# Kernel optimization log

Hardware: AMD Instinct MI355X
Metric: run time of the kernel (lower is better)

## Reference

```python
import jax, jax.numpy as jnp
import numpy as np

H = 2048          # hidden_size
I = 768           # moe_intermediate_size
E = 64            # num_experts
TOP_K = 8         # num_experts_per_tok (norm_topk_prob=True)
B, S = 1, 1024


def setup_inputs() -> dict:
    key = jax.random.key(0)
    ks = jax.random.split(key, 5)
    scale = 0.02
    return {
        "hidden_states": jax.random.normal(ks[0], (B, S, H), dtype=jnp.float32),
        "W_router": jax.random.normal(ks[1], (H, E), dtype=jnp.float32) * scale,
        "W_gate": jax.random.normal(ks[2], (E, H, I), dtype=jnp.float32) * scale,
        "W_up": jax.random.normal(ks[3], (E, H, I), dtype=jnp.float32) * scale,
        "W_down": jax.random.normal(ks[4], (E, I, H), dtype=jnp.float32) * scale,
    }


def reference(hidden_states, W_router, W_gate, W_up, W_down):
    b, s, h = hidden_states.shape
    x = hidden_states.reshape(-1, h)                      # [T, H]

    # --- Qwen3MoeTopKRouter: linear gate -> fp32 softmax -> top-k -> renorm ---
    logits = x @ W_router                                 # [T, E]
    probs = jax.nn.softmax(logits.astype(jnp.float32), axis=-1)
    top_w, top_idx = jax.lax.top_k(probs, TOP_K)          # [T, K]
    top_w = top_w / jnp.sum(top_w, axis=-1, keepdims=True)  # norm_topk_prob
    top_w = top_w.astype(x.dtype)

    # combine weights per (token, expert): zero if expert not selected
    comb = jnp.sum(jax.nn.one_hot(top_idx, E, dtype=x.dtype) * top_w[..., None], axis=1)  # [T, E]

    # --- per-expert SwiGLU MLP: down(silu(gate(x)) * up(x)), dense-masked ---
    g = jnp.einsum('th,ehi->eti', x, W_gate)              # [E, T, I]
    u = jnp.einsum('th,ehi->eti', x, W_up)                # [E, T, I]
    hmid = jax.nn.silu(g) * u                             # [E, T, I]
    # fold combine weight into the intermediate to avoid an [E, T, H] buffer
    hmid = hmid * comb.T[:, :, None]                      # [E, T, I]
    out = jnp.einsum('eti,eih->th', hmid, W_down)         # [T, H]

    return out.reshape(b, s, h)
```

## Files before the change

kernel.cpp:

```cpp
#include <hip/hip_runtime.h>
#include <hip/hip_bf16.h>

#define H_DIM 2048
#define I_DIM 768
#define NEXP 64
#define TOPK 8
#define NTOK 1024
#define BM 256
#define BKS 32

typedef float f32x4 __attribute__((ext_vector_type(4)));
typedef float f32x2 __attribute__((ext_vector_type(2)));
typedef unsigned int u32x4 __attribute__((ext_vector_type(4)));
typedef short bf16v8 __attribute__((ext_vector_type(8)));
typedef unsigned int u32;


__device__ inline unsigned short f2bf(float f) {
    union { float f; u32 u; } v; v.f = f;
    u32 r = (v.u + 0x7FFFu + ((v.u >> 16) & 1u)) >> 16;
    return (unsigned short)r;
}
__device__ inline u32 pack2(float a, float b) {
    return (u32)f2bf(a) | ((u32)f2bf(b) << 16);
}

__global__ void zero_kernel(float4* p, int n4) {
    int i = blockIdx.x * blockDim.x + threadIdx.x;
    if (i < n4) p[i] = (float4){0.f, 0.f, 0.f, 0.f};
}

__global__ void xconv_kernel(const float4* __restrict__ x, ushort4* __restrict__ xbf, int n4) {
    int i = blockIdx.x * blockDim.x + threadIdx.x;
    if (i < n4) {
        float4 v = x[i];
        ushort4 o;
        o.x = f2bf(v.x); o.y = f2bf(v.y); o.z = f2bf(v.z); o.w = f2bf(v.w);
        xbf[i] = o;
    }
}

__global__ __launch_bounds__(64) void router_kernel(
    const float* __restrict__ x, const float* __restrict__ Wr,
    int* __restrict__ topk_idx, float* __restrict__ topk_w)
{
    const int t = blockIdx.x;
    const int e = threadIdx.x;
    __shared__ float xs[H_DIM];

    const float* xrow = x + (size_t)t * H_DIM;
    #pragma unroll
    for (int m = 0; m < H_DIM / 64; ++m) xs[m * 64 + e] = xrow[m * 64 + e];
    __syncthreads();

    float acc = 0.f;
    #pragma unroll 8
    for (int h = 0; h < H_DIM; ++h) acc += xs[h] * Wr[(size_t)h * NEXP + e];

    float m = acc;
    #pragma unroll
    for (int o = 32; o > 0; o >>= 1) m = fmaxf(m, __shfl_xor(m, o));
    float p = __expf(acc - m);
    float s = p;
    #pragma unroll
    for (int o = 32; o > 0; o >>= 1) s += __shfl_xor(s, o);
    float prob = p / s;

    float myp = prob;
    float kw[TOPK]; int kid[TOPK]; float wsum = 0.f;
    #pragma unroll
    for (int k = 0; k < TOPK; ++k) {
        float v = myp; int bi = e;
        #pragma unroll
        for (int o = 32; o > 0; o >>= 1) {
            float ov = __shfl_xor(v, o);
            int   oi = __shfl_xor(bi, o);
            if (ov > v || (ov == v && oi < bi)) { v = ov; bi = oi; }
        }
        kw[k] = v; kid[k] = bi; wsum += v;
        if (e == bi) myp = -1.f;
    }
    if (e == 0) {
        float inv = 1.f / wsum;
        #pragma unroll
        for (int k = 0; k < TOPK; ++k) {
            topk_idx[t * TOPK + k] = kid[k];
            topk_w[t * TOPK + k]   = kw[k] * inv;
        }
    }
}

__global__ __launch_bounds__(64) void listbuild_kernel(
    const int* __restrict__ topk_idx, const float* __restrict__ topk_w,
    int* __restrict__ counts, int* __restrict__ lists, float* __restrict__ wlist)
{
    const int e = blockIdx.x;
    const int lane = threadIdx.x;
    int n = 0;
    for (int base = 0; base < NTOK * TOPK; base += 64) {
        int s = base + lane;
        int idx = topk_idx[s];
        bool match = (idx == e);
        unsigned long long mask = __ballot(match);
        int pre = __popcll(mask & ((1ull << lane) - 1ull));
        if (match) {
            lists[e * NTOK + n + pre] = s >> 3;
            wlist[e * NTOK + n + pre] = topk_w[s];
        }
        n += __popcll(mask);
    }
    if (lane == 0) counts[e] = n;
}

__global__ __launch_bounds__(64) void scan_kernel(
    const int* __restrict__ counts, int* __restrict__ offsets)
{
    int e = threadIdx.x;
    int v = counts[e];
    int xacc = v;
    #pragma unroll
    for (int o = 1; o < 64; o <<= 1) {
        int y = __shfl_up(xacc, o);
        if (e >= o) xacc += y;
    }
    offsets[e] = xacc - v;
}

__global__ __launch_bounds__(512) void gateup_kernel(
    const unsigned short* __restrict__ xbf,
    const float* __restrict__ Wg, const float* __restrict__ Wu,
    const int* __restrict__ counts, const int* __restrict__ offsets,
    const int* __restrict__ lists, const float* __restrict__ wlist,
    unsigned short* __restrict__ hmid)
{
    const int b  = blockIdx.x;
    const int wg = (b & 7) * 96 + (b >> 3);
    const int itile = wg % 12;
    const int e     = wg / 12;

    const int count = counts[e];
    if (count == 0) return;
    const int off = offsets[e];
    const int i0 = itile * 64;

    __shared__ unsigned short Alds[BM][40];
    __shared__ u32 Bgl[64 * 20];
    __shared__ u32 Bul[64 * 20];

    const int tid  = threadIdx.x;
    const int lane = tid & 63;
    const int wid  = tid >> 6;
    const int wm   = wid >> 1, wn = wid & 1;
    const int kb   = lane >> 4;
    const int l15  = lane & 15;

    const float* WgE = Wg + (size_t)e * H_DIM * I_DIM + i0;
    const float* WuE = Wu + (size_t)e * H_DIM * I_DIM + i0;

    const int bn  = (tid & 31) * 2;
    const int bkp = tid >> 5;
    const int ar  = tid >> 1;
    const int ah  = (tid & 1) * 16;

    for (int mstart = 0; mstart < count; mstart += BM) {
        const int pr = mstart + ar;
        const bool aact = pr < count;
        const unsigned short* xrow = xbf + (size_t)(aact ? lists[e * NTOK + pr] : 0) * H_DIM + ah;
        const bool mact = (mstart + wm * 64) < count;

        f32x4 accg[4][2], accu[4][2];
        #pragma unroll
        for (int i = 0; i < 4; ++i)
            #pragma unroll
            for (int j = 0; j < 2; ++j) {
                accg[i][j] = (f32x4){0.f, 0.f, 0.f, 0.f};
                accu[i][j] = (f32x4){0.f, 0.f, 0.f, 0.f};
            }

        u32x4 pA0, pA1;
        f32x2 g0a, g1a, u0a, u1a;
        f32x2 g0b, g1b, u0b, u1b;

#define LOADA(h)                                                                \
        if (aact) {                                                             \
            const u32x4* pa_ = (const u32x4*)(xrow + (h));                      \
            pA0 = pa_[0]; pA1 = pa_[1];                                         \
        }
#define LOADB(G0,G1,U0,U1,h)                                                    \
        {                                                                       \
            G0 = __builtin_nontemporal_load((const f32x2*)(WgE + (size_t)((h) + 2 * bkp)     * I_DIM + bn)); \
            G1 = __builtin_nontemporal_load((const f32x2*)(WgE + (size_t)((h) + 2 * bkp + 1) * I_DIM + bn)); \
            U0 = __builtin_nontemporal_load((const f32x2*)(WuE + (size_t)((h) + 2 * bkp)     * I_DIM + bn)); \
            U1 = __builtin_nontemporal_load((const f32x2*)(WuE + (size_t)((h) + 2 * bkp + 1) * I_DIM + bn)); \
        }
#define STOREA()                                                                \
        if (aact) {                                                             \
            *(u32x4*)&Alds[ar][ah]     = pA0;                                   \
            *(u32x4*)&Alds[ar][ah + 8] = pA1;                                   \
        }
#define STOREB(G0,G1,U0,U1)                                                     \
        {                                                                       \
            Bgl[(bn)     * 20 + bkp] = pack2(G0.x, G1.x);                       \
            Bgl[(bn + 1) * 20 + bkp] = pack2(G0.y, G1.y);                       \
            Bul[(bn)     * 20 + bkp] = pack2(U0.x, U1.x);                       \
            Bul[(bn + 1) * 20 + bkp] = pack2(U0.y, U1.y);                       \
        }
#define MFMA_PHASE()                                                            \
        if (mact) {                                                             \
            bf16v8 af[4], bg[2], bu[2];                                         \
            _Pragma("unroll")                                                   \
            for (int mf = 0; mf < 4; ++mf)                                      \
                af[mf] = *(const bf16v8*)&Alds[wm * 64 + mf * 16 + l15][kb * 8];\
            _Pragma("unroll")                                                   \
            for (int nf = 0; nf < 2; ++nf) {                                    \
                int n = wn * 32 + nf * 16 + l15;                                \
                bg[nf] = *(const bf16v8*)&Bgl[n * 20 + kb * 4];                 \
                bu[nf] = *(const bf16v8*)&Bul[n * 20 + kb * 4];                 \
            }                                                                   \
            _Pragma("unroll")                                                   \
            for (int mf = 0; mf < 4; ++mf)                                      \
                _Pragma("unroll")                                               \
                for (int nf = 0; nf < 2; ++nf) {                                \
                    accg[mf][nf] = __builtin_amdgcn_mfma_f32_16x16x32_bf16(af[mf], bg[nf], accg[mf][nf], 0, 0, 0); \
                    accu[mf][nf] = __builtin_amdgcn_mfma_f32_16x16x32_bf16(af[mf], bu[nf], accu[mf][nf], 0, 0, 0); \
                }                                                               \
        }

        LOADB(g0a, g1a, u0a, u1a, 0);
        LOADB(g0b, g1b, u0b, u1b, BKS);
        LOADA(0);

        for (int hh = 0; hh < H_DIM; hh += 2 * BKS) {
            STOREA(); STOREB(g0a, g1a, u0a, u1a);
            __syncthreads();
            if (hh + 2 * BKS < H_DIM) LOADB(g0a, g1a, u0a, u1a, hh + 2 * BKS);
            LOADA(hh + BKS);
            MFMA_PHASE();
            __syncthreads();
            STOREA(); STOREB(g0b, g1b, u0b, u1b);
            __syncthreads();
            if (hh + 3 * BKS < H_DIM) LOADB(g0b, g1b, u0b, u1b, hh + 3 * BKS);
            if (hh + 2 * BKS < H_DIM) LOADA(hh + 2 * BKS);
            MFMA_PHASE();
            __syncthreads();
        }
#undef LOADA
#undef LOADB
#undef STOREA
#undef STOREB
#undef MFMA_PHASE

        if (mact) {
            #pragma unroll
            for (int mf = 0; mf < 4; ++mf)
                #pragma unroll
                for (int nf = 0; nf < 2; ++nf)
                    #pragma unroll
                    for (int r = 0; r < 4; ++r) {
                        int ml  = wm * 64 + mf * 16 + (lane >> 4) * 4 + r;
                        int pos = mstart + ml;
                        if (pos < count) {
                            float wgt = wlist[e * NTOK + pos];
                            float g = accg[mf][nf][r], u = accu[mf][nf][r];
                            float s = 1.f / (1.f + __expf(-g));
                            float h = g * s * u * wgt;
                            hmid[(size_t)(off + pos) * I_DIM + i0 + wn * 32 + nf * 16 + l15] = f2bf(h);
                        }
                    }
        }
    }
}

__global__ __launch_bounds__(512) void down_kernel(
    const unsigned short* __restrict__ hmid, const float* __restrict__ Wd,
    const int* __restrict__ counts, const int* __restrict__ offsets,
    const int* __restrict__ lists, float* __restrict__ out)
{
    const int b  = blockIdx.x;
    const int wg = (b & 7) * 256 + (b >> 3);
    const int htile = wg % 32;
    const int e     = wg / 32;

    const int count = counts[e];
    if (count == 0) return;
    const int off = offsets[e];
    const int h0 = htile * 64;

    __shared__ unsigned short Alds[BM][40];
    __shared__ u32 Bdl[64 * 20];

    const int tid  = threadIdx.x;
    const int lane = tid & 63;
    const int wid  = tid >> 6;
    const int wm   = wid >> 1, wn = wid & 1;
    const int kb   = lane >> 4;
    const int l15  = lane & 15;

    const float* WdE = Wd + (size_t)e * I_DIM * H_DIM + h0;

    const int bn  = (tid & 31) * 2;
    const int bkp = tid >> 5;
    const int ar  = tid >> 1;
    const int ah  = (tid & 1) * 16;

    for (int mstart = 0; mstart < count; mstart += BM) {
        const int pr = mstart + ar;
        const bool aact = pr < count;
        const unsigned short* hrow = hmid + (size_t)(off + (aact ? pr : 0)) * I_DIM + ah;
        const bool mact = (mstart + wm * 64) < count;

        f32x4 acc[4][2];
        #pragma unroll
        for (int i = 0; i < 4; ++i)
            #pragma unroll
            for (int j = 0; j < 2; ++j) acc[i][j] = (f32x4){0.f, 0.f, 0.f, 0.f};

        u32x4 pH0, pH1;
        f32x2 d0a, d1a, d0b, d1b;

#define LOADA(k)                                                                \
        if (aact) {                                                             \
            const u32x4* p_ = (const u32x4*)(hrow + (k));                       \
            pH0 = p_[0]; pH1 = p_[1];                                           \
        }
#define LOADB(D0,D1,k)                                                          \
        {                                                                       \
            D0 = __builtin_nontemporal_load((const f32x2*)(WdE + (size_t)((k) + 2 * bkp)     * H_DIM + bn)); \
            D1 = __builtin_nontemporal_load((const f32x2*)(WdE + (size_t)((k) + 2 * bkp + 1) * H_DIM + bn)); \
        }
#define STOREA()                                                                \
        if (aact) {                                                             \
            *(u32x4*)&Alds[ar][ah]     = pH0;                                   \
            *(u32x4*)&Alds[ar][ah + 8] = pH1;                                   \
        }
#define STOREB(D0,D1)                                                           \
        {                                                                       \
            Bdl[(bn)     * 20 + bkp] = pack2(D0.x, D1.x);                       \
            Bdl[(bn + 1) * 20 + bkp] = pack2(D0.y, D1.y);                       \
        }
#define MFMA_PHASE()                                                            \
        if (mact) {                                                             \
            bf16v8 af[4], bd[2];                                                \
            _Pragma("unroll")                                                   \
            for (int mf = 0; mf < 4; ++mf)                                      \
                af[mf] = *(const bf16v8*)&Alds[wm * 64 + mf * 16 + l15][kb * 8];\
            _Pragma("unroll")                                                   \
            for (int nf = 0; nf < 2; ++nf) {                                    \
                int n = wn * 32 + nf * 16 + l15;                                \
                bd[nf] = *(const bf16v8*)&Bdl[n * 20 + kb * 4];                 \
            }                                                                   \
            _Pragma("unroll")                                                   \
            for (int mf = 0; mf < 4; ++mf)                                      \
                _Pragma("unroll")                                               \
                for (int nf = 0; nf < 2; ++nf)                                  \
                    acc[mf][nf] = __builtin_amdgcn_mfma_f32_16x16x32_bf16(af[mf], bd[nf], acc[mf][nf], 0, 0, 0); \
        }

        LOADB(d0a, d1a, 0);
        LOADB(d0b, d1b, BKS);
        LOADA(0);

        for (int ii = 0; ii < I_DIM; ii += 2 * BKS) {
            STOREA(); STOREB(d0a, d1a);
            __syncthreads();
            if (ii + 2 * BKS < I_DIM) LOADB(d0a, d1a, ii + 2 * BKS);
            LOADA(ii + BKS);
            MFMA_PHASE();
            __syncthreads();

            STOREA(); STOREB(d0b, d1b);
            __syncthreads();
            if (ii + 3 * BKS < I_DIM) LOADB(d0b, d1b, ii + 3 * BKS);
            if (ii + 2 * BKS < I_DIM) LOADA(ii + 2 * BKS);
            MFMA_PHASE();
            __syncthreads();
        }
#undef LOADA
#undef LOADB
#undef STOREA
#undef STOREB
#undef MFMA_PHASE

        if (mact) {
            #pragma unroll
            for (int mf = 0; mf < 4; ++mf)
                #pragma unroll
                for (int nf = 0; nf < 2; ++nf)
                    #pragma unroll
                    for (int r = 0; r < 4; ++r) {
                        int ml  = wm * 64 + mf * 16 + (lane >> 4) * 4 + r;
                        int pos = mstart + ml;
                        if (pos < count) {
                            int tok = lists[e * NTOK + pos];
                            atomicAdd(&out[(size_t)tok * H_DIM + h0 + wn * 32 + nf * 16 + l15],
                                      acc[mf][nf][r]);
                        }
                    }
        }
    }
}

extern "C" void kernel_launch(void* const* d_in, const int* in_sizes, int n_in,
                              void* d_out, int out_size, void* d_ws, size_t ws_size,
                              hipStream_t stream) {
    const float* x  = (const float*)d_in[0];
    const float* Wr = (const float*)d_in[1];
    const float* Wg = (const float*)d_in[2];
    const float* Wu = (const float*)d_in[3];
    const float* Wd = (const float*)d_in[4];
    float* out = (float*)d_out;

    char* ws = (char*)d_ws;
    int*   topk_idx = (int*)  (ws + 0);
    float* topk_w   = (float*)(ws + 32768);
    int*   counts   = (int*)  (ws + 65536);
    int*   offsets  = (int*)  (ws + 65792);
    int*   lists    = (int*)  (ws + 66048);
    float* wlist    = (float*)(ws + 328192);
    unsigned short* hmid = (unsigned short*)(ws + 590336);
    unsigned short* xbf  = (unsigned short*)(ws + 13173248);

    const int nout4 = NTOK * H_DIM / 4;
    hipLaunchKernelGGL(zero_kernel, dim3((nout4 + 255) / 256), dim3(256), 0, stream,
                       (float4*)out, nout4);
    hipLaunchKernelGGL(xconv_kernel, dim3((NTOK * H_DIM / 4 + 255) / 256), dim3(256), 0, stream,
                       (const float4*)x, (ushort4*)xbf, NTOK * H_DIM / 4);
    hipLaunchKernelGGL(router_kernel, dim3(NTOK), dim3(64), 0, stream,
                       x, Wr, topk_idx, topk_w);
    hipLaunchKernelGGL(listbuild_kernel, dim3(NEXP), dim3(64), 0, stream,
                       topk_idx, topk_w, counts, lists, wlist);
    hipLaunchKernelGGL(scan_kernel, dim3(1), dim3(64), 0, stream,
                       counts, offsets);
    hipLaunchKernelGGL(gateup_kernel, dim3(12 * NEXP), dim3(512), 0, stream,
                       xbf, Wg, Wu, counts, offsets, lists, wlist, hmid);
    hipLaunchKernelGGL(down_kernel, dim3(32 * NEXP), dim3(512), 0, stream,
                       hmid, Wd, counts, offsets, lists, out);
}
```

Measured before the change: 561.4 us.

## Halve N-tile width in MoE GEMMs and swizzle B LDS layout

```diff
diff --git a/kernel.cpp b/kernel.cpp
--- a/kernel.cpp
+++ b/kernel.cpp
@@ -12,6 +12,7 @@
 typedef float f32x4 __attribute__((ext_vector_type(4)));
 typedef float f32x2 __attribute__((ext_vector_type(2)));
 typedef unsigned int u32x4 __attribute__((ext_vector_type(4)));
+typedef unsigned int u32x2 __attribute__((ext_vector_type(2)));
 typedef short bf16v8 __attribute__((ext_vector_type(8)));
 typedef unsigned int u32;
 
@@ -134,18 +135,18 @@
     unsigned short* __restrict__ hmid)
 {
     const int b  = blockIdx.x;
-    const int wg = (b & 7) * 96 + (b >> 3);
-    const int itile = wg % 12;
-    const int e     = wg / 12;
+    const int wg = (b & 7) * 192 + (b >> 3);
+    const int itile = wg % 24;
+    const int e     = wg / 24;
 
     const int count = counts[e];
     if (count == 0) return;
     const int off = offsets[e];
-    const int i0 = itile * 64;
+    const int i0 = itile * 32;
 
     __shared__ unsigned short Alds[BM][40];
-    __shared__ u32 Bgl[64 * 20];
-    __shared__ u32 Bul[64 * 20];
+    __shared__ u32 Bgl[32 * 20];
+    __shared__ u32 Bul[32 * 20];
 
     const int tid  = threadIdx.x;
     const int lane = tid & 63;
@@ -157,10 +158,16 @@
     const float* WgE = Wg + (size_t)e * H_DIM * I_DIM + i0;
     const float* WuE = Wu + (size_t)e * H_DIM * I_DIM + i0;
 
-    const int bn  = (tid & 31) * 2;
-    const int bkp = tid >> 5;
-    const int ar  = tid >> 1;
-    const int ah  = (tid & 1) * 16;
+    const int ar = tid >> 1;
+    const int ah = (tid & 1) * 16;
+    const int bnn  = tid & 31;
+    const int bkq  = (tid >> 5) & 7;
+    const int bmat = tid >> 8;
+    const float* WB = bmat ? WuE : WgE;
+    const int key4w = 4 * ((bnn >> 3) & 3);
+    u32* bdst = (bmat ? Bul : Bgl) + bnn * 20 + ((2 * bkq) ^ key4w);
+    const int brn   = wn * 16 + l15;
+    const int key4r = 4 * ((brn >> 3) & 3);
 
     for (int mstart = 0; mstart < count; mstart += BM) {
         const int pr = mstart + ar;
@@ -168,78 +175,69 @@
         const unsigned short* xrow = xbf + (size_t)(aact ? lists[e * NTOK + pr] : 0) * H_DIM + ah;
         const bool mact = (mstart + wm * 64) < count;
 
-        f32x4 accg[4][2], accu[4][2];
+        f32x4 accg[4], accu[4];
         #pragma unroll
-        for (int i = 0; i < 4; ++i)
-            #pragma unroll
-            for (int j = 0; j < 2; ++j) {
-                accg[i][j] = (f32x4){0.f, 0.f, 0.f, 0.f};
-                accu[i][j] = (f32x4){0.f, 0.f, 0.f, 0.f};
-            }
+        for (int i = 0; i < 4; ++i) {
+            accg[i] = (f32x4){0.f, 0.f, 0.f, 0.f};
+            accu[i] = (f32x4){0.f, 0.f, 0.f, 0.f};
+        }
 
         u32x4 pA0, pA1;
-        f32x2 g0a, g1a, u0a, u1a;
-        f32x2 g0b, g1b, u0b, u1b;
+        float b0a, b1a, b2a, b3a;
+        float b0b, b1b, b2b, b3b;
 
 #define LOADA(h)                                                                \
         if (aact) {                                                             \
             const u32x4* pa_ = (const u32x4*)(xrow + (h));                      \
             pA0 = pa_[0]; pA1 = pa_[1];                                         \
         }
-#define LOADB(G0,G1,U0,U1,h)                                                    \
+#define LOADB(R0,R1,R2,R3,h)                                                    \
         {                                                                       \
-            G0 = __builtin_nontemporal_load((const f32x2*)(WgE + (size_t)((h) + 2 * bkp)     * I_DIM + bn)); \
-            G1 = __builtin_nontemporal_load((const f32x2*)(WgE + (size_t)((h) + 2 * bkp + 1) * I_DIM + bn)); \
-            U0 = __builtin_nontemporal_load((const f32x2*)(WuE + (size_t)((h) + 2 * bkp)     * I_DIM + bn)); \
-            U1 = __builtin_nontemporal_load((const f32x2*)(WuE + (size_t)((h) + 2 * bkp + 1) * I_DIM + bn)); \
+            R0 = __builtin_nontemporal_load(WB + (size_t)((h) + 4 * bkq)     * I_DIM + bnn); \
+            R1 = __builtin_nontemporal_load(WB + (size_t)((h) + 4 * bkq + 1) * I_DIM + bnn); \
+            R2 = __builtin_nontemporal_load(WB + (size_t)((h) + 4 * bkq + 2) * I_DIM + bnn); \
+            R3 = __builtin_nontemporal_load(WB + (size_t)((h) + 4 * bkq + 3) * I_DIM + bnn); \
         }
 #define STOREA()                                                                \
         if (aact) {                                                             \
             *(u32x4*)&Alds[ar][ah]     = pA0;                                   \
             *(u32x4*)&Alds[ar][ah + 8] = pA1;                                   \
         }
-#define STOREB(G0,G1,U0,U1)                                                     \
+#define STOREB(R0,R1,R2,R3)                                                     \
         {                                                                       \
-            Bgl[(bn)     * 20 + bkp] = pack2(G0.x, G1.x);                       \
-            Bgl[(bn + 1) * 20 + bkp] = pack2(G0.y, G1.y);                       \
-            Bul[(bn)     * 20 + bkp] = pack2(U0.x, U1.x);                       \
-            Bul[(bn + 1) * 20 + bkp] = pack2(U0.y, U1.y);                       \
+            u32x2 w_; w_.x = pack2(R0, R1); w_.y = pack2(R2, R3);               \
+            *(u32x2*)bdst = w_;                                                 \
         }
 #define MFMA_PHASE()                                                            \
         if (mact) {                                                             \
-            bf16v8 af[4], bg[2], bu[2];                                         \
+            bf16v8 af[4], bg, bu;                                               \
             _Pragma("unroll")                                                   \
             for (int mf = 0; mf < 4; ++mf)                                      \
                 af[mf] = *(const bf16v8*)&Alds[wm * 64 + mf * 16 + l15][kb * 8];\
+            bg = *(const bf16v8*)&Bgl[brn * 20 + ((4 * kb) ^ key4r)];           \
+            bu = *(const bf16v8*)&Bul[brn * 20 + ((4 * kb) ^ key4r)];           \
             _Pragma("unroll")                                                   \
-            for (int nf = 0; nf < 2; ++nf) {                                    \
-                int n = wn * 32 + nf * 16 + l15;                                \
-                bg[nf] = *(const bf16v8*)&Bgl[n * 20 + kb * 4];                 \
-                bu[nf] = *(const bf16v8*)&Bul[n * 20 + kb * 4];                 \
+            for (int mf = 0; mf < 4; ++mf) {                                    \
+                accg[mf] = __builtin_amdgcn_mfma_f32_16x16x32_bf16(af[mf], bg, accg[mf], 0, 0, 0); \
+                accu[mf] = __builtin_amdgcn_mfma_f32_16x16x32_bf16(af[mf], bu, accu[mf], 0, 0, 0); \
             }                                                                   \
-            _Pragma("unroll")                                                   \
-            for (int mf = 0; mf < 4; ++mf)                                      \
-                _Pragma("unroll")                                               \
-                for (int nf = 0; nf < 2; ++nf) {                                \
-                    accg[mf][nf] = __builtin_amdgcn_mfma_f32_16x16x32_bf16(af[mf], bg[nf], accg[mf][nf], 0, 0, 0); \
-                    accu[mf][nf] = __builtin_amdgcn_mfma_f32_16x16x32_bf16(af[mf], bu[nf], accu[mf][nf], 0, 0, 0); \
-                }                                                               \
-        }
-
-        LOADB(g0a, g1a, u0a, u1a, 0);
-        LOADB(g0b, g1b, u0b, u1b, BKS);
+        }
+
+        LOADB(b0a, b1a, b2a, b3a, 0);
+        LOADB(b0b, b1b, b2b, b3b, BKS);
         LOADA(0);
 
         for (int hh = 0; hh < H_DIM; hh += 2 * BKS) {
-            STOREA(); STOREB(g0a, g1a, u0a, u1a);
-            __syncthreads();
-            if (hh + 2 * BKS < H_DIM) LOADB(g0a, g1a, u0a, u1a, hh + 2 * BKS);
+            STOREA(); STOREB(b0a, b1a, b2a, b3a);
+            __syncthreads();
+            if (hh + 2 * BKS < H_DIM) LOADB(b0a, b1a, b2a, b3a, hh + 2 * BKS);
             LOADA(hh + BKS);
             MFMA_PHASE();
             __syncthreads();
-            STOREA(); STOREB(g0b, g1b, u0b, u1b);
-            __syncthreads();
-            if (hh + 3 * BKS < H_DIM) LOADB(g0b, g1b, u0b, u1b, hh + 3 * BKS);
+
+            STOREA(); STOREB(b0b, b1b, b2b, b3b);
+            __syncthreads();
+            if (hh + 3 * BKS < H_DIM) LOADB(b0b, b1b, b2b, b3b, hh + 3 * BKS);
             if (hh + 2 * BKS < H_DIM) LOADA(hh + 2 * BKS);
             MFMA_PHASE();
             __syncthreads();
@@ -254,19 +252,16 @@
             #pragma unroll
             for (int mf = 0; mf < 4; ++mf)
                 #pragma unroll
-                for (int nf = 0; nf < 2; ++nf)
-                    #pragma unroll
-                    for (int r = 0; r < 4; ++r) {
-                        int ml  = wm * 64 + mf * 16 + (lane >> 4) * 4 + r;
-                        int pos = mstart + ml;
-                        if (pos < count) {
-                            float wgt = wlist[e * NTOK + pos];
-                            float g = accg[mf][nf][r], u = accu[mf][nf][r];
-                            float s = 1.f / (1.f + __expf(-g));
-                            float h = g * s * u * wgt;
-                            hmid[(size_t)(off + pos) * I_DIM + i0 + wn * 32 + nf * 16 + l15] = f2bf(h);
-                        }
+                for (int r = 0; r < 4; ++r) {
+                    int pos = mstart + wm * 64 + mf * 16 + kb * 4 + r;
+                    if (pos < count) {
+                        float wgt = wlist[e * NTOK + pos];
+                        float g = accg[mf][r], u = accu[mf][r];
+                        float s = 1.f / (1.f + __expf(-g));
+                        float h = g * s * u * wgt;
+                        hmid[(size_t)(off + pos) * I_DIM + i0 + wn * 16 + l15] = f2bf(h);
                     }
+                }
         }
     }
 }
@@ -277,17 +272,17 @@
     const int* __restrict__ lists, float* __restrict__ out)
 {
     const int b  = blockIdx.x;
-    const int wg = (b & 7) * 256 + (b >> 3);
-    const int htile = wg % 32;
-    const int e     = wg / 32;
+    const int wg = (b & 7) * 512 + (b >> 3);
+    const int htile = wg % 64;
+    const int e     = wg / 64;
 
     const int count = counts[e];
     if (count == 0) return;
     const int off = offsets[e];
-    const int h0 = htile * 64;
+    const int h0 = htile * 32;
 
     __shared__ unsigned short Alds[BM][40];
-    __shared__ u32 Bdl[64 * 20];
+    __shared__ u32 Bdl[32 * 20];
 
     const int tid  = threadIdx.x;
     const int lane = tid & 63;
@@ -298,10 +293,15 @@
 
     const float* WdE = Wd + (size_t)e * I_DIM * H_DIM + h0;
 
-    const int bn  = (tid & 31) * 2;
-    const int bkp = tid >> 5;
-    const int ar  = tid >> 1;
-    const int ah  = (tid & 1) * 16;
+    const int ar = tid >> 1;
+    const int ah = (tid & 1) * 16;
+    const int bnn  = tid & 31;
+    const int bkq  = (tid >> 5) & 7;
+    const bool bact = tid < 256;
+    const int key4w = 4 * ((bnn >> 3) & 3);
+    u32* bdst = Bdl + bnn * 20 + ((2 * bkq) ^ key4w);
+    const int brn   = wn * 16 + l15;
+    const int key4r = 4 * ((brn >> 3) & 3);
 
     for (int mstart = 0; mstart < count; mstart += BM) {
         const int pr = mstart + ar;
@@ -309,68 +309,63 @@
         const unsigned short* hrow = hmid + (size_t)(off + (aact ? pr : 0)) * I_DIM + ah;
         const bool mact = (mstart + wm * 64) < count;
 
-        f32x4 acc[4][2];
+        f32x4 acc[4];
         #pragma unroll
-        for (int i = 0; i < 4; ++i)
-            #pragma unroll
-            for (int j = 0; j < 2; ++j) acc[i][j] = (f32x4){0.f, 0.f, 0.f, 0.f};
+        for (int i = 0; i < 4; ++i) acc[i] = (f32x4){0.f, 0.f, 0.f, 0.f};
 
         u32x4 pH0, pH1;
-        f32x2 d0a, d1a, d0b, d1b;
+        float d0a, d1a, d2a, d3a;
+        float d0b, d1b, d2b, d3b;
 
 #define LOADA(k)                                                                \
         if (aact) {                                                             \
             const u32x4* p_ = (const u32x4*)(hrow + (k));                       \
             pH0 = p_[0]; pH1 = p_[1];                                           \
         }
-#define LOADB(D0,D1,k)                                                          \
-        {                                                                       \
-            D0 = __builtin_nontemporal_load((const f32x2*)(WdE + (size_t)((k) + 2 * bkp)     * H_DIM + bn)); \
-            D1 = __builtin_nontemporal_load((const f32x2*)(WdE + (size_t)((k) + 2 * bkp + 1) * H_DIM + bn)); \
+#define LOADB(R0,R1,R2,R3,k)                                                    \
+        if (bact) {                                                             \
+            R0 = __builtin_nontemporal_load(WdE + (size_t)((k) + 4 * bkq)     * H_DIM + bnn); \
+            R1 = __builtin_nontemporal_load(WdE + (size_t)((k) + 4 * bkq + 1) * H_DIM + bnn); \
+            R2 = __builtin_nontemporal_load(WdE + (size_t)((k) + 4 * bkq + 2) * H_DIM + bnn); \
+            R3 = __builtin_nontemporal_load(WdE + (size_t)((k) + 4 * bkq + 3) * H_DIM + bnn); \
         }
 #define STOREA()                                                                \
         if (aact) {                                                             \
             *(u32x4*)&Alds[ar][ah]     = pH0;                                   \
             *(u32x4*)&Alds[ar][ah + 8] = pH1;                                   \
         }
-#define STOREB(D0,D1)                                                           \
-        {                                                                       \
-            Bdl[(bn)     * 20 + bkp] = pack2(D0.x, D1.x);                       \
-            Bdl[(bn + 1) * 20 + bkp] = pack2(D0.y, D1.y);                       \
+#define STOREB(R0,R1,R2,R3)                                                     \
+        if (bact) {                                                             \
+            u32x2 w_; w_.x = pack2(R0, R1); w_.y = pack2(R2, R3);               \
+            *(u32x2*)bdst = w_;                                                 \
         }
 #define MFMA_PHASE()                                                            \
         if (mact) {                                                             \
-            bf16v8 af[4], bd[2];                                                \
+            bf16v8 af[4], bd;                                                   \
             _Pragma("unroll")                                                   \
             for (int mf = 0; mf < 4; ++mf)                                      \
                 af[mf] = *(const bf16v8*)&Alds[wm * 64 + mf * 16 + l15][kb * 8];\
-            _Pragma("unroll")                                                   \
-            for (int nf = 0; nf < 2; ++nf) {                                    \
-                int n = wn * 32 + nf * 16 + l15;                                \
-                bd[nf] = *(const bf16v8*)&Bdl[n * 20 + kb * 4];                 \
-            }                                                                   \
+            bd = *(const bf16v8*)&Bdl[brn * 20 + ((4 * kb) ^ key4r)];           \
             _Pragma("unroll")                                                   \
             for (int mf = 0; mf < 4; ++mf)                                      \
-                _Pragma("unroll")                                               \
-                for (int nf = 0; nf < 2; ++nf)                                  \
-                    acc[mf][nf] = __builtin_amdgcn_mfma_f32_16x16x32_bf16(af[mf], bd[nf], acc[mf][nf], 0, 0, 0); \
-        }
-
-        LOADB(d0a, d1a, 0);
-        LOADB(d0b, d1b, BKS);
+                acc[mf] = __builtin_amdgcn_mfma_f32_16x16x32_bf16(af[mf], bd, acc[mf], 0, 0, 0); \
+        }
+
+        LOADB(d0a, d1a, d2a, d3a, 0);
+        LOADB(d0b, d1b, d2b, d3b, BKS);
         LOADA(0);
 
         for (int ii = 0; ii < I_DIM; ii += 2 * BKS) {
-            STOREA(); STOREB(d0a, d1a);
-            __syncthreads();
-            if (ii + 2 * BKS < I_DIM) LOADB(d0a, d1a, ii + 2 * BKS);
+            STOREA(); STOREB(d0a, d1a, d2a, d3a);
+            __syncthreads();
+            if (ii + 2 * BKS < I_DIM) LOADB(d0a, d1a, d2a, d3a, ii + 2 * BKS);
             LOADA(ii + BKS);
             MFMA_PHASE();
             __syncthreads();
 
-            STOREA(); STOREB(d0b, d1b);
-            __syncthreads();
-            if (ii + 3 * BKS < I_DIM) LOADB(d0b, d1b, ii + 3 * BKS);
+            STOREA(); STOREB(d0b, d1b, d2b, d3b);
+            __syncthreads();
+            if (ii + 3 * BKS < I_DIM) LOADB(d0b, d1b, d2b, d3b, ii + 3 * BKS);
             if (ii + 2 * BKS < I_DIM) LOADA(ii + 2 * BKS);
             MFMA_PHASE();
             __syncthreads();
@@ -385,17 +380,14 @@
             #pragma unroll
             for (int mf = 0; mf < 4; ++mf)
                 #pragma unroll
-                for (int nf = 0; nf < 2; ++nf)
-                    #pragma unroll
-                    for (int r = 0; r < 4; ++r) {
-                        int ml  = wm * 64 + mf * 16 + (lane >> 4) * 4 + r;
-                        int pos = mstart + ml;
-                        if (pos < count) {
-                            int tok = lists[e * NTOK + pos];
-                            atomicAdd(&out[(size_t)tok * H_DIM + h0 + wn * 32 + nf * 16 + l15],
-                                      acc[mf][nf][r]);
-                        }
+                for (int r = 0; r < 4; ++r) {
+                    int pos = mstart + wm * 64 + mf * 16 + kb * 4 + r;
+                    if (pos < count) {
+                        int tok = lists[e * NTOK + pos];
+                        atomicAdd(&out[(size_t)tok * H_DIM + h0 + wn * 16 + l15],
+                                  acc[mf][r]);
                     }
+                }
         }
     }
 }
@@ -431,8 +423,8 @@
                        topk_idx, topk_w, counts, lists, wlist);
     hipLaunchKernelGGL(scan_kernel, dim3(1), dim3(64), 0, stream,
                        counts, offsets);
-    hipLaunchKernelGGL(gateup_kernel, dim3(12 * NEXP), dim3(512), 0, stream,
+    hipLaunchKernelGGL(gateup_kernel, dim3(24 * NEXP), dim3(512), 0, stream,
                        xbf, Wg, Wu, counts, offsets, lists, wlist, hmid);
-    hipLaunchKernelGGL(down_kernel, dim3(32 * NEXP), dim3(512), 0, stream,
+    hipLaunchKernelGGL(down_kernel, dim3(64 * NEXP), dim3(512), 0, stream,
                        hmid, Wd, counts, offsets, lists, out);
 }
```

Measured after the change: 568.0 us. About the same (+1.2%).
